# Kernel optimization log

Hardware: AMD Instinct MI355X
Metric: run time of the kernel (lower is better)

The kernel has to match this reference:

```python
import jax, jax.numpy as jnp
import numpy as np

D_K = 64


def setup_inputs() -> dict:
    key = jax.random.key(0)
    kq, kk, kv = jax.random.split(key, 3)
    B, H, S, D = 2, 16, 2048, D_K
    Q = jax.random.normal(kq, (B, H, S, D), dtype=jnp.float32)
    K = jax.random.normal(kk, (B, H, S, D), dtype=jnp.float32)
    V = jax.random.normal(kv, (B, H, S, D), dtype=jnp.float32)
    # causal mask: True = masked out (matches torch masked_fill_ semantics)
    causal = ~jnp.tril(jnp.ones((S, S), dtype=bool))
    attn_mask = jnp.broadcast_to(causal, (B, 1, S, S))
    return {"Q": Q, "K": K, "V": V, "attn_mask": attn_mask}


def reference(Q, K, V, attn_mask):
    # scores = Q K^T / sqrt(d_k), masked positions -> -1e9, softmax, then A V
    scale = 1.0 / np.sqrt(D_K).astype(np.float32)
    scores = jnp.einsum("bhqd,bhkd->bhqk", Q, K) * scale
    scores = jnp.where(attn_mask, jnp.float32(-1e9), scores)
    attn = jax.nn.softmax(scores, axis=-1)
    context = jnp.einsum("bhqk,bhkd->bhqd", attn, V)
    return (context, attn)
```

## Files before the change

### kernel.cpp

```cpp
#include <hip/hip_runtime.h>

typedef _Float16 half8  __attribute__((ext_vector_type(8)));
typedef _Float16 half4v __attribute__((ext_vector_type(4)));
typedef float    f32x4  __attribute__((ext_vector_type(4)));

#define S_LEN  2048
#define D_HEAD 64
#define TQ     16
#define EBS    2056

static __device__ __forceinline__ half8 cvt8(float4 a, float4 b) {
    half8 h;
    h[0] = (_Float16)a.x; h[1] = (_Float16)a.y; h[2] = (_Float16)a.z; h[3] = (_Float16)a.w;
    h[4] = (_Float16)b.x; h[5] = (_Float16)b.y; h[6] = (_Float16)b.z; h[7] = (_Float16)b.w;
    return h;
}

__global__ void prep_k(const float* __restrict__ K, _Float16* __restrict__ Kh, int n8) {
    int i = blockIdx.x * blockDim.x + threadIdx.x;
    if (i < n8) {
        const float4* p = (const float4*)K + (size_t)i * 2;
        ((half8*)Kh)[i] = cvt8(p[0], p[1]);
    }
}

__global__ void prep_vt(const float* __restrict__ V, _Float16* __restrict__ Vt) {
    __shared__ _Float16 lt[D_HEAD][136];
    const int bh = blockIdx.y;
    const int k0 = blockIdx.x * 128;
    const int t  = threadIdx.x;
    {
        const int kk = t >> 1, hf = t & 1;
        const float* vp = V + (size_t)bh * S_LEN * D_HEAD + (size_t)(k0 + kk) * D_HEAD + hf * 32;
#pragma unroll
        for (int j = 0; j < 8; ++j) {
            float4 a = *(const float4*)(vp + j * 4);
            lt[hf * 32 + j * 4 + 0][kk] = (_Float16)a.x;
            lt[hf * 32 + j * 4 + 1][kk] = (_Float16)a.y;
            lt[hf * 32 + j * 4 + 2][kk] = (_Float16)a.z;
            lt[hf * 32 + j * 4 + 3][kk] = (_Float16)a.w;
        }
    }
    __syncthreads();
    {
        const int d = t >> 2, kq = t & 3;
        _Float16* dst = Vt + ((size_t)bh * D_HEAD + d) * S_LEN + k0 + kq * 32;
        const half8* src = (const half8*)&lt[d][kq * 32];
#pragma unroll
        for (int j = 0; j < 4; ++j) ((half8*)dst)[j] = src[j];
    }
}

template <bool USE_WS>
__global__ __launch_bounds__(256, 2)
void sdpa_main(const float* __restrict__ Q, const float* __restrict__ K,
               const _Float16* __restrict__ Kh, const float* __restrict__ V,
               const _Float16* __restrict__ Vt, float* __restrict__ ctx,
               float* __restrict__ attn) {
    __shared__ __align__(16) _Float16 ebuf[TQ][EBS];
    __shared__ float rowsum[TQ];
    __shared__ float inv_l[TQ];

    const int tid  = threadIdx.x;
    const int wave = tid >> 6;
    const int lane = tid & 63;
    const int c    = lane & 15;
    const int quad = lane >> 4;

    const int qt = blockIdx.x;
    const int bh = blockIdx.y;
    const int q0 = qt * TQ;
    const int n_k   = q0 + TQ;
    const int n_t16 = n_k >> 4;
    const int n_c32 = (n_k + 31) >> 5;

    const size_t base = (size_t)bh * (S_LEN * D_HEAD);

    if (tid < TQ) rowsum[tid] = 0.0f;
    if (n_k & 31) {
        int r = tid >> 4, kk = n_k + (tid & 15);
        ebuf[r][kk] = (_Float16)0.0f;
    }

    half8 qf0, qf1;
    {
        const float* qp = Q + base + (size_t)(q0 + c) * D_HEAD + quad * 8;
        qf0 = cvt8(*(const float4*)qp, *(const float4*)(qp + 4));
        qf1 = cvt8(*(const float4*)(qp + 32), *(const float4*)(qp + 36));
    }
    __syncthreads();

    float psum = 0.0f;
    for (int t = wave; t < n_t16; t += 4) {
        const int k0 = t * 16;
        half8 kf0, kf1;
        if (USE_WS) {
            const _Float16* kp = Kh + base + (size_t)(k0 + c) * D_HEAD + quad * 8;
            kf0 = *(const half8*)kp;
            kf1 = *(const half8*)(kp + 32);
        } else {
            const float* kp = K + base + (size_t)(k0 + c) * D_HEAD + quad * 8;
            kf0 = cvt8(*(const float4*)kp, *(const float4*)(kp + 4));
            kf1 = cvt8(*(const float4*)(kp + 32), *(const float4*)(kp + 36));
        }
        f32x4 s = {0.0f, 0.0f, 0.0f, 0.0f};
        s = __builtin_amdgcn_mfma_f32_16x16x32_f16(kf0, qf0, s, 0, 0, 0);
        s = __builtin_amdgcn_mfma_f32_16x16x32_f16(kf1, qf1, s, 0, 0, 0);

        half4v ev;
#pragma unroll
        for (int r = 0; r < 4; ++r) {
            const int kg = k0 + quad * 4 + r;
            float e = (kg <= q0 + c) ? __expf(s[r] * 0.125f) : 0.0f;
            psum += e;
            ev[r] = (_Float16)e;
        }
        *(half4v*)&ebuf[c][k0 + quad * 4] = ev;
    }
    psum += __shfl_xor(psum, 16);
    psum += __shfl_xor(psum, 32);
    if (lane < 16) atomicAdd(&rowsum[c], psum);
    __syncthreads();
    if (tid < TQ) inv_l[tid] = 1.0f / rowsum[tid];

    f32x4 cacc = {0.0f, 0.0f, 0.0f, 0.0f};
    if (USE_WS) {
        const _Float16* vb = Vt + ((size_t)bh * D_HEAD + wave * 16 + c) * S_LEN;
        for (int chk = 0; chk < n_c32; ++chk) {
            const int k0 = chk * 32;
            half8 af = *(const half8*)&ebuf[c][k0 + quad * 8];
            half8 bf = *(const half8*)(vb + k0 + quad * 8);
            cacc = __builtin_amdgcn_mfma_f32_16x16x32_f16(af, bf, cacc, 0, 0, 0);
        }
    } else {
        for (int chk = 0; chk < n_c32; ++chk) {
            const int k0 = chk * 32;
            half8 af = *(const half8*)&ebuf[c][k0 + quad * 8];
            half8 bf;
#pragma unroll
            for (int j = 0; j < 8; ++j)
                bf[j] = (_Float16)V[base + (size_t)(k0 + quad * 8 + j) * D_HEAD + wave * 16 + c];
            cacc = __builtin_amdgcn_mfma_f32_16x16x32_f16(af, bf, cacc, 0, 0, 0);
        }
    }
    __syncthreads();

    {
        const int r  = tid >> 4;
        const int qg = q0 + r;
        const float il = inv_l[r];
        float* row = attn + (size_t)bh * S_LEN * S_LEN + (size_t)(q0 + r) * S_LEN;
#pragma unroll
        for (int it = 0; it < 16; ++it) {
            const int k8 = (tid & 15) * 8 + it * 128;
            float4 o0, o1;
            if (k8 + 7 <= qg) {
                half8 e = *(const half8*)&ebuf[r][k8];
                o0.x = (float)e[0] * il; o0.y = (float)e[1] * il;
                o0.z = (float)e[2] * il; o0.w = (float)e[3] * il;
                o1.x = (float)e[4] * il; o1.y = (float)e[5] * il;
                o1.z = (float)e[6] * il; o1.w = (float)e[7] * il;
            } else if (k8 > qg) {
                o0.x = o0.y = o0.z = o0.w = 0.0f;
                o1 = o0;
            } else {
                half8 e = *(const half8*)&ebuf[r][k8];
                o0.x = (k8 + 0 <= qg) ? (float)e[0] * il : 0.0f;
                o0.y = (k8 + 1 <= qg) ? (float)e[1] * il : 0.0f;
                o0.z = (k8 + 2 <= qg) ? (float)e[2] * il : 0.0f;
                o0.w = (k8 + 3 <= qg) ? (float)e[3] * il : 0.0f;
                o1.x = (k8 + 4 <= qg) ? (float)e[4] * il : 0.0f;
                o1.y = (k8 + 5 <= qg) ? (float)e[5] * il : 0.0f;
                o1.z = (k8 + 6 <= qg) ? (float)e[6] * il : 0.0f;
                o1.w = (k8 + 7 <= qg) ? (float)e[7] * il : 0.0f;
            }
            *(float4*)(row + k8)     = o0;
            *(float4*)(row + k8 + 4) = o1;
        }
    }

#pragma unroll
    for (int r = 0; r < 4; ++r) {
        const int qr = quad * 4 + r;
        ctx[base + (size_t)(q0 + qr) * D_HEAD + wave * 16 + c] = cacc[r] * inv_l[qr];
    }
}

extern "C" void kernel_launch(void* const* d_in, const int* in_sizes, int n_in,
                              void* d_out, int out_size, void* d_ws, size_t ws_size,
                              hipStream_t stream) {
    const float* Q = (const float*)d_in[0];
    const float* K = (const float*)d_in[1];
    const float* V = (const float*)d_in[2];

    const int BH = in_sizes[0] / (S_LEN * D_HEAD);
    float* ctx  = (float*)d_out;
    float* attn = (float*)d_out + (size_t)in_sizes[0];

    const size_t nKV  = (size_t)in_sizes[1];
    const size_t need = 2 * nKV * sizeof(_Float16);

    dim3 grid(S_LEN / TQ, BH);
    if (ws_size >= need) {
        _Float16* Kh = (_Float16*)d_ws;
        _Float16* Vt = Kh + nKV;
        prep_k<<<(int)((nKV / 8 + 255) / 256), 256, 0, stream>>>(K, Kh, (int)(nKV / 8));
        prep_vt<<<dim3(S_LEN / 128, BH), 256, 0, stream>>>(V, Vt);
        sdpa_main<true><<<grid, 256, 0, stream>>>(Q, K, Kh, V, Vt, ctx, attn);
    } else {
        sdpa_main<false><<<grid, 256, 0, stream>>>(Q, K, nullptr, V, nullptr, ctx, attn);
    }
}
```

Before: 743.5 us.

## Recompute QK^T in a second pass and fuse softmax output with PV

Drops the shared-memory exponent buffer and its block-wide synchronisation. Each wave now owns 16 query rows and makes two passes over the keys: the first pass only accumulates the row sum, the second recomputes the scores, writes the normalised probabilities straight to global memory and feeds them into 16x16x16 MFMAs against transposed V. Blocks cover 64 query rows and are ordered in zigzag pairs to balance causal work, and launch bounds allow higher occupancy. The cost is doubled QK^T compute and K loads, plus attention stores that are scattered across 16 rows per instruction rather than contiguous row segments.

Measured after the change: 972.0 us. 30.7% more time.

```diff
diff --git a/kernel.cpp b/kernel.cpp
--- a/kernel.cpp
+++ b/kernel.cpp
@@ -1,13 +1,12 @@
 #include <hip/hip_runtime.h>
 
-typedef _Float16 half8  __attribute__((ext_vector_type(8)));
-typedef _Float16 half4v __attribute__((ext_vector_type(4)));
-typedef float    f32x4  __attribute__((ext_vector_type(4)));
+typedef _Float16 half8 __attribute__((ext_vector_type(8)));
+typedef _Float16 half4 __attribute__((ext_vector_type(4)));
+typedef float    f32x4 __attribute__((ext_vector_type(4)));
 
 #define S_LEN  2048
 #define D_HEAD 64
-#define TQ     16
-#define EBS    2056
+#define NT16   (S_LEN / 16)
 
 static __device__ __forceinline__ half8 cvt8(float4 a, float4 b) {
     half8 h;
@@ -52,46 +51,37 @@
 }
 
 template <bool USE_WS>
-__global__ __launch_bounds__(256, 2)
+__global__ __launch_bounds__(256, 4)
 void sdpa_main(const float* __restrict__ Q, const float* __restrict__ K,
                const _Float16* __restrict__ Kh, const float* __restrict__ V,
                const _Float16* __restrict__ Vt, float* __restrict__ ctx,
                float* __restrict__ attn) {
-    __shared__ __align__(16) _Float16 ebuf[TQ][EBS];
-    __shared__ float rowsum[TQ];
-    __shared__ float inv_l[TQ];
-
     const int tid  = threadIdx.x;
     const int wave = tid >> 6;
     const int lane = tid & 63;
     const int c    = lane & 15;
     const int quad = lane >> 4;
 
-    const int qt = blockIdx.x;
+    const int x  = blockIdx.x;
+    const int qt = (x & 1) ? (31 - (x >> 1)) : (x >> 1);
     const int bh = blockIdx.y;
-    const int q0 = qt * TQ;
-    const int n_k   = q0 + TQ;
-    const int n_t16 = n_k >> 4;
-    const int n_c32 = (n_k + 31) >> 5;
+
+    const int q0w   = qt * 64 + wave * 16;
+    const int qg    = q0w + c;
+    const int tdiag = q0w >> 4;
 
     const size_t base = (size_t)bh * (S_LEN * D_HEAD);
 
-    if (tid < TQ) rowsum[tid] = 0.0f;
-    if (n_k & 31) {
-        int r = tid >> 4, kk = n_k + (tid & 15);
-        ebuf[r][kk] = (_Float16)0.0f;
-    }
-
     half8 qf0, qf1;
     {
-        const float* qp = Q + base + (size_t)(q0 + c) * D_HEAD + quad * 8;
+        const float* qp = Q + base + (size_t)qg * D_HEAD + quad * 8;
         qf0 = cvt8(*(const float4*)qp, *(const float4*)(qp + 4));
         qf1 = cvt8(*(const float4*)(qp + 32), *(const float4*)(qp + 36));
     }
-    __syncthreads();
 
     float psum = 0.0f;
-    for (int t = wave; t < n_t16; t += 4) {
+#pragma unroll 2
+    for (int t = 0; t <= tdiag; ++t) {
         const int k0 = t * 16;
         half8 kf0, kf1;
         if (USE_WS) {
@@ -106,84 +96,84 @@
         f32x4 s = {0.0f, 0.0f, 0.0f, 0.0f};
         s = __builtin_amdgcn_mfma_f32_16x16x32_f16(kf0, qf0, s, 0, 0, 0);
         s = __builtin_amdgcn_mfma_f32_16x16x32_f16(kf1, qf1, s, 0, 0, 0);
-
-        half4v ev;
 #pragma unroll
         for (int r = 0; r < 4; ++r) {
             const int kg = k0 + quad * 4 + r;
-            float e = (kg <= q0 + c) ? __expf(s[r] * 0.125f) : 0.0f;
-            psum += e;
-            ev[r] = (_Float16)e;
-        }
-        *(half4v*)&ebuf[c][k0 + quad * 4] = ev;
+            if (kg <= qg) psum += __expf(s[r] * 0.125f);
+        }
     }
     psum += __shfl_xor(psum, 16);
     psum += __shfl_xor(psum, 32);
-    if (lane < 16) atomicAdd(&rowsum[c], psum);
-    __syncthreads();
-    if (tid < TQ) inv_l[tid] = 1.0f / rowsum[tid];
-
-    f32x4 cacc = {0.0f, 0.0f, 0.0f, 0.0f};
-    if (USE_WS) {
-        const _Float16* vb = Vt + ((size_t)bh * D_HEAD + wave * 16 + c) * S_LEN;
-        for (int chk = 0; chk < n_c32; ++chk) {
-            const int k0 = chk * 32;
-            half8 af = *(const half8*)&ebuf[c][k0 + quad * 8];
-            half8 bf = *(const half8*)(vb + k0 + quad * 8);
-            cacc = __builtin_amdgcn_mfma_f32_16x16x32_f16(af, bf, cacc, 0, 0, 0);
-        }
-    } else {
-        for (int chk = 0; chk < n_c32; ++chk) {
-            const int k0 = chk * 32;
-            half8 af = *(const half8*)&ebuf[c][k0 + quad * 8];
-            half8 bf;
-#pragma unroll
-            for (int j = 0; j < 8; ++j)
-                bf[j] = (_Float16)V[base + (size_t)(k0 + quad * 8 + j) * D_HEAD + wave * 16 + c];
-            cacc = __builtin_amdgcn_mfma_f32_16x16x32_f16(af, bf, cacc, 0, 0, 0);
-        }
-    }
-    __syncthreads();
-
-    {
-        const int r  = tid >> 4;
-        const int qg = q0 + r;
-        const float il = inv_l[r];
-        float* row = attn + (size_t)bh * S_LEN * S_LEN + (size_t)(q0 + r) * S_LEN;
-#pragma unroll
-        for (int it = 0; it < 16; ++it) {
-            const int k8 = (tid & 15) * 8 + it * 128;
-            float4 o0, o1;
-            if (k8 + 7 <= qg) {
-                half8 e = *(const half8*)&ebuf[r][k8];
-                o0.x = (float)e[0] * il; o0.y = (float)e[1] * il;
-                o0.z = (float)e[2] * il; o0.w = (float)e[3] * il;
-                o1.x = (float)e[4] * il; o1.y = (float)e[5] * il;
-                o1.z = (float)e[6] * il; o1.w = (float)e[7] * il;
-            } else if (k8 > qg) {
-                o0.x = o0.y = o0.z = o0.w = 0.0f;
-                o1 = o0;
-            } else {
-                half8 e = *(const half8*)&ebuf[r][k8];
-                o0.x = (k8 + 0 <= qg) ? (float)e[0] * il : 0.0f;
-                o0.y = (k8 + 1 <= qg) ? (float)e[1] * il : 0.0f;
-                o0.z = (k8 + 2 <= qg) ? (float)e[2] * il : 0.0f;
-                o0.w = (k8 + 3 <= qg) ? (float)e[3] * il : 0.0f;
-                o1.x = (k8 + 4 <= qg) ? (float)e[4] * il : 0.0f;
-                o1.y = (k8 + 5 <= qg) ? (float)e[5] * il : 0.0f;
-                o1.z = (k8 + 6 <= qg) ? (float)e[6] * il : 0.0f;
-                o1.w = (k8 + 7 <= qg) ? (float)e[7] * il : 0.0f;
+    const float inv = 1.0f / psum;
+
+    f32x4 cacc[4] = {{0,0,0,0}, {0,0,0,0}, {0,0,0,0}, {0,0,0,0}};
+    float* rowp = attn + ((size_t)bh * S_LEN + qg) * S_LEN;
+    const _Float16* vb0 = Vt + ((size_t)bh * D_HEAD + 0  + c) * S_LEN;
+    const _Float16* vb1 = Vt + ((size_t)bh * D_HEAD + 16 + c) * S_LEN;
+    const _Float16* vb2 = Vt + ((size_t)bh * D_HEAD + 32 + c) * S_LEN;
+    const _Float16* vb3 = Vt + ((size_t)bh * D_HEAD + 48 + c) * S_LEN;
+
+#pragma unroll 2
+    for (int t = 0; t <= tdiag; ++t) {
+        const int k0 = t * 16;
+        half8 kf0, kf1;
+        if (USE_WS) {
+            const _Float16* kp = Kh + base + (size_t)(k0 + c) * D_HEAD + quad * 8;
+            kf0 = *(const half8*)kp;
+            kf1 = *(const half8*)(kp + 32);
+        } else {
+            const float* kp = K + base + (size_t)(k0 + c) * D_HEAD + quad * 8;
+            kf0 = cvt8(*(const float4*)kp, *(const float4*)(kp + 4));
+            kf1 = cvt8(*(const float4*)(kp + 32), *(const float4*)(kp + 36));
+        }
+        f32x4 s = {0.0f, 0.0f, 0.0f, 0.0f};
+        s = __builtin_amdgcn_mfma_f32_16x16x32_f16(kf0, qf0, s, 0, 0, 0);
+        s = __builtin_amdgcn_mfma_f32_16x16x32_f16(kf1, qf1, s, 0, 0, 0);
+
+        float4 o;
+        half4  a4;
+#pragma unroll
+        for (int r = 0; r < 4; ++r) {
+            const int kg = k0 + quad * 4 + r;
+            float p = (kg <= qg) ? __expf(s[r] * 0.125f) * inv : 0.0f;
+            ((float*)&o)[r] = p;
+            a4[r] = (_Float16)p;
+        }
+        *(float4*)(rowp + k0 + quad * 4) = o;
+
+        const int kq = k0 + quad * 4;
+        half4 b0 = *(const half4*)(vb0 + kq);
+        half4 b1 = *(const half4*)(vb1 + kq);
+        half4 b2 = *(const half4*)(vb2 + kq);
+        half4 b3 = *(const half4*)(vb3 + kq);
+        if (USE_WS) {
+            cacc[0] = __builtin_amdgcn_mfma_f32_16x16x16f16(a4, b0, cacc[0], 0, 0, 0);
+            cacc[1] = __builtin_amdgcn_mfma_f32_16x16x16f16(a4, b1, cacc[1], 0, 0, 0);
+            cacc[2] = __builtin_amdgcn_mfma_f32_16x16x16f16(a4, b2, cacc[2], 0, 0, 0);
+            cacc[3] = __builtin_amdgcn_mfma_f32_16x16x16f16(a4, b3, cacc[3], 0, 0, 0);
+        } else {
+#pragma unroll
+            for (int g = 0; g < 4; ++g) {
+                half4 bg;
+#pragma unroll
+                for (int j = 0; j < 4; ++j)
+                    bg[j] = (_Float16)V[base + (size_t)(kq + j) * D_HEAD + g * 16 + c];
+                cacc[g] = __builtin_amdgcn_mfma_f32_16x16x16f16(a4, bg, cacc[g], 0, 0, 0);
             }
-            *(float4*)(row + k8)     = o0;
-            *(float4*)(row + k8 + 4) = o1;
-        }
-    }
-
-#pragma unroll
-    for (int r = 0; r < 4; ++r) {
-        const int qr = quad * 4 + r;
-        ctx[base + (size_t)(q0 + qr) * D_HEAD + wave * 16 + c] = cacc[r] * inv_l[qr];
-    }
+        }
+    }
+
+    {
+        const float4 z = {0.0f, 0.0f, 0.0f, 0.0f};
+        for (int t = tdiag + 1; t < NT16; ++t)
+            *(float4*)(rowp + t * 16 + quad * 4) = z;
+    }
+
+#pragma unroll
+    for (int g = 0; g < 4; ++g)
+#pragma unroll
+        for (int r = 0; r < 4; ++r)
+            ctx[base + (size_t)(q0w + quad * 4 + r) * D_HEAD + g * 16 + c] = cacc[g][r];
 }
 
 extern "C" void kernel_launch(void* const* d_in, const int* in_sizes, int n_in,
@@ -200,7 +190,7 @@
     const size_t nKV  = (size_t)in_sizes[1];
     const size_t need = 2 * nKV * sizeof(_Float16);
 
-    dim3 grid(S_LEN / TQ, BH);
+    dim3 grid(S_LEN / 64, BH);
     if (ws_size >= need) {
         _Float16* Kh = (_Float16*)d_ws;
         _Float16* Vt = Kh + nKV;
```
